# Kernel tuning notes

Measured on AMD Instinct MI355X. Metric: run time of the kernel, lower is better.

The kernel has to match this reference:

```python
import jax, jax.numpy as jnp
import numpy as np

N_NODES = 100000
N_EDGES = 1600000
DIM_IN = 128
DIM_OUT = 128


def setup_inputs() -> dict:
    key = jax.random.key(0)
    k1, k2, k3, k4, k5 = jax.random.split(key, 5)
    x = jax.random.normal(k1, (N_NODES, DIM_IN), dtype=jnp.float32)
    # Dense kernel (glorot-style scale)
    W = jax.random.normal(k2, (DIM_IN, DIM_OUT), dtype=jnp.float32) * (1.0 / np.sqrt(DIM_IN))
    edge_vals = jax.random.uniform(k3, (N_EDGES,), dtype=jnp.float32)
    edge_rows = jax.random.randint(k4, (N_EDGES,), 0, N_NODES, dtype=jnp.int32)
    edge_cols = jax.random.randint(k5, (N_EDGES,), 0, N_NODES, dtype=jnp.int32)
    return {"x": x, "W": W, "edge_vals": edge_vals,
            "edge_rows": edge_rows, "edge_cols": edge_cols}


def reference(x, W, edge_vals, edge_rows, edge_cols):
    # Dense projection (Dense, use_bias=False): [N, dim_in] @ [dim_in, dim_out]
    h = x @ W
    # Sparse adjacency SpMM in COO form:
    # out[r] = sum_{edges e with row r} vals[e] * h[col[e]]
    msgs = edge_vals[:, None] * h[edge_cols]            # [E, dim_out]
    out = jax.ops.segment_sum(msgs, edge_rows, num_segments=N_NODES)
    return out
```

## Files before the change

### kernel.cpp

```cpp
#include <hip/hip_runtime.h>
#include <hip/hip_bf16.h>
#include <hip/hip_fp16.h>


#define DIM 128
#define RB 128
#define NB_MAX 1024
#define CH 4096
#define REG_CAP 2560

typedef short s16x8 __attribute__((ext_vector_type(8)));
typedef float f32x4 __attribute__((ext_vector_type(4)));
typedef unsigned short u16;
typedef unsigned long long u64;
typedef u16 u16x4 __attribute__((ext_vector_type(4)));
typedef u16 u16x8 __attribute__((ext_vector_type(8)));

static __device__ __forceinline__ u16 f2bf(float f) {
  union { float f; unsigned u; } a; a.f = f;
  return (u16)((a.u + 0x7fffu + ((a.u >> 16) & 1u)) >> 16);
}
static __device__ __forceinline__ float bf_lo(unsigned u) {
  union { unsigned u; float f; } a; a.u = u << 16; return a.f;
}
static __device__ __forceinline__ float bf_hi(unsigned u) {
  union { unsigned u; float f; } a; a.u = u & 0xffff0000u; return a.f;
}
static __device__ __forceinline__ u16 f2h(float f) {
  return __half_as_ushort(__float2half(f));
}
static __device__ __forceinline__ float h2f(u16 h) {
  return __half2float(__ushort_as_half(h));
}

__global__ __launch_bounds__(256) void repack_w_kernel(
    const float* __restrict__ W, u16* __restrict__ Wp) {
  int e = blockIdx.x * 256 + threadIdx.x;
  int k = e >> 7, n = e & 127;
  Wp[((k >> 3) * 128 + n) * 8 + (k & 7)] = f2bf(W[e]);
}

__global__ __launch_bounds__(256) void mfma_gemm_kernel(
    const float* __restrict__ x, const u16* __restrict__ Wp,
    u16* __restrict__ hb, int n_nodes) {
  __shared__ u16 xl[128 * 136];
  const int t = threadIdx.x;
  const int m0 = blockIdx.x * 128;

  const float4* x4 = (const float4*)x;
#pragma unroll
  for (int it = 0; it < 16; ++it) {
    int i = it * 256 + t;
    int r = i >> 5, c = i & 31;
    float4 v = make_float4(0.f, 0.f, 0.f, 0.f);
    int node = m0 + r;
    if (node < n_nodes) v = x4[(size_t)node * 32 + c];
    u16x4 pk = {f2bf(v.x), f2bf(v.y), f2bf(v.z), f2bf(v.w)};
    *(u16x4*)&xl[r * 136 + c * 4] = pk;
  }
  __syncthreads();

  const int w = t >> 6, l = t & 63, q = l >> 4, n15 = l & 15;

  f32x4 acc[2][8];
#pragma unroll
  for (int mt = 0; mt < 2; ++mt)
#pragma unroll
    for (int nt = 0; nt < 8; ++nt) acc[mt][nt] = (f32x4){0.f, 0.f, 0.f, 0.f};

#pragma unroll
  for (int ks = 0; ks < 4; ++ks) {
    s16x8 a0 = *(const s16x8*)&xl[(w * 32 + n15) * 136 + ks * 32 + q * 8];
    s16x8 a1 = *(const s16x8*)&xl[(w * 32 + 16 + n15) * 136 + ks * 32 + q * 8];
#pragma unroll
    for (int nt = 0; nt < 8; ++nt) {
      s16x8 b = *(const s16x8*)&Wp[(size_t)(((ks * 4 + q) * 128) + nt * 16 + n15) * 8];
      acc[0][nt] = __builtin_amdgcn_mfma_f32_16x16x32_bf16(a0, b, acc[0][nt], 0, 0, 0);
      acc[1][nt] = __builtin_amdgcn_mfma_f32_16x16x32_bf16(a1, b, acc[1][nt], 0, 0, 0);
    }
  }
  __syncthreads();

#pragma unroll
  for (int mt = 0; mt < 2; ++mt)
#pragma unroll
    for (int nt = 0; nt < 8; ++nt)
#pragma unroll
      for (int r_ = 0; r_ < 4; ++r_)
        xl[(w * 32 + mt * 16 + q * 4 + r_) * 136 + nt * 16 + n15] =
            f2bf(acc[mt][nt][r_]);
  __syncthreads();

#pragma unroll
  for (int it = 0; it < 8; ++it) {
    int chunk = it * 256 + t;
    int r = chunk >> 4, c = chunk & 15;
    int node = m0 + r;
    if (node < n_nodes)
      *(u16x8*)(hb + (size_t)node * 128 + c * 8) = *(const u16x8*)&xl[r * 136 + c * 8];
  }
}

__global__ __launch_bounds__(256) void part_kernel(
    const int* __restrict__ rows, const int* __restrict__ cols,
    const float* __restrict__ vals, int* __restrict__ gcur,
    u64* __restrict__ reg, int n_edges, int nb) {
  __shared__ int hist[NB_MAX];
  __shared__ int ofs[NB_MAX];
  __shared__ int gbase[NB_MAX];
  __shared__ int lcur[NB_MAX];
  __shared__ int tsum[256];
  __shared__ u64 srec[CH];

  const int t = threadIdx.x;
  const int base = blockIdx.x * CH;

  for (int i = t; i < NB_MAX; i += 256) { hist[i] = 0; lcur[i] = 0; }
  __syncthreads();

  int r[16], c[16];
  float v[16];
  bool ok[16];
#pragma unroll
  for (int i = 0; i < 16; ++i) {
    int e = base + i * 256 + t;
    ok[i] = e < n_edges;
    r[i] = ok[i] ? rows[e] : 0;
    c[i] = ok[i] ? cols[e] : 0;
    v[i] = ok[i] ? vals[e] : 0.f;
    if (ok[i]) atomicAdd(&hist[r[i] >> 7], 1);
  }
  __syncthreads();

  const int b0 = t * 4;
  int h0 = hist[b0], h1 = hist[b0 + 1], h2 = hist[b0 + 2], h3 = hist[b0 + 3];
  int run = h0 + h1 + h2 + h3;
  tsum[t] = run;
  for (int b = t; b < nb; b += 256) {
    int hc = hist[b];
    gbase[b] = (hc > 0) ? atomicAdd(&gcur[b], hc) : 0;
  }
  __syncthreads();
  for (int off = 1; off < 256; off <<= 1) {
    int x = (t >= off) ? tsum[t - off] : 0;
    __syncthreads();
    tsum[t] += x;
    __syncthreads();
  }
  int ex = tsum[t] - run;
  ofs[b0] = ex;
  ofs[b0 + 1] = ex + h0;
  ofs[b0 + 2] = ex + h0 + h1;
  ofs[b0 + 3] = ex + h0 + h1 + h2;
  __syncthreads();

#pragma unroll
  for (int i = 0; i < 16; ++i) {
    if (ok[i]) {
      int bkt = r[i] >> 7;
      int pos = ofs[bkt] + atomicAdd(&lcur[bkt], 1);
      srec[pos] = ((u64)(unsigned)r[i] << 33) | ((u64)(unsigned)c[i] << 16) |
                  (u64)f2h(v[i]);
    }
  }
  __syncthreads();

  int nvalid = n_edges - base;
  if (nvalid > CH) nvalid = CH;
  for (int i = t; i < nvalid; i += 256) {
    u64 rec = srec[i];
    int row = (int)(rec >> 33);
    int bkt = row >> 7;
    int dst = gbase[bkt] + (i - ofs[bkt]);
    if (dst < REG_CAP) reg[(size_t)bkt * REG_CAP + dst] = rec;
  }
}

__global__ __launch_bounds__(1024) void bucket_accum_kernel(
    const u16* __restrict__ hb, const u64* __restrict__ reg,
    const int* __restrict__ gcur, float* __restrict__ out, int n_nodes) {
  __shared__ int hist[RB];
  __shared__ int ofs[RB];
  __shared__ int lcur[RB];
  __shared__ u64 srt[REG_CAP];

  const int t = threadIdx.x;
  const int b = blockIdx.x;
  const int row0 = b * RB;

  int n_e = gcur[b];
  if (n_e > REG_CAP) n_e = REG_CAP;

  if (t < RB) { hist[t] = 0; lcur[t] = 0; }
  __syncthreads();

  u64 rr[3];
  int rl[3];
  bool ok[3];
#pragma unroll
  for (int i = 0; i < 3; ++i) {
    int j = i * 1024 + t;
    ok[i] = j < n_e;
    rr[i] = ok[i] ? reg[(size_t)b * REG_CAP + j] : 0;
    rl[i] = (int)(rr[i] >> 33) & (RB - 1);
    if (ok[i]) atomicAdd(&hist[rl[i]], 1);
  }
  __syncthreads();

  if (t < 64) {
    int h0 = hist[2 * t], h1 = hist[2 * t + 1];
    int s = h0 + h1;
    int v = s;
#pragma unroll
    for (int off = 1; off < 64; off <<= 1) {
      int u = __shfl_up(v, off, 64);
      if (t >= off) v += u;
    }
    int ex = v - s;
    ofs[2 * t] = ex;
    ofs[2 * t + 1] = ex + h0;
  }
  __syncthreads();

#pragma unroll
  for (int i = 0; i < 3; ++i) {
    if (ok[i]) {
      int pos = ofs[rl[i]] + atomicAdd(&lcur[rl[i]], 1);
      srt[pos] = rr[i];
    }
  }
  __syncthreads();

  const int lane = t & 63;
  const int w = t >> 6;
  const unsigned* h32 = (const unsigned*)hb;
  float2* out2 = (float2*)out;

  for (int k = 0; k < RB / 16; ++k) {
    int rli = w * (RB / 16) + k;
    int gr = row0 + rli;
    if (gr >= n_nodes) continue;
    int s = ofs[rli];
    int n = hist[rli];
    float2 acc = make_float2(0.f, 0.f);
    int i = 0;
    for (; i + 8 <= n; i += 8) {
      unsigned uu[8];
      float vv[8];
#pragma unroll
      for (int j = 0; j < 8; ++j) {
        u64 rec = srt[s + i + j];
        int col = (int)((rec >> 16) & 0x1FFFF);
        vv[j] = h2f((u16)(rec & 0xFFFF));
        uu[j] = h32[(size_t)col * 64 + lane];
      }
#pragma unroll
      for (int j = 0; j < 8; ++j) {
        acc.x += vv[j] * bf_lo(uu[j]);
        acc.y += vv[j] * bf_hi(uu[j]);
      }
    }
    for (; i < n; ++i) {
      u64 rec = srt[s + i];
      int col = (int)((rec >> 16) & 0x1FFFF);
      float vv = h2f((u16)(rec & 0xFFFF));
      unsigned uu = h32[(size_t)col * 64 + lane];
      acc.x += vv * bf_lo(uu);
      acc.y += vv * bf_hi(uu);
    }
    out2[(size_t)gr * 64 + lane] = acc;
  }
}

__global__ __launch_bounds__(256) void scatter_kernel(
    const u16* __restrict__ hb, const float* __restrict__ vals,
    const int* __restrict__ rows, const int* __restrict__ cols,
    float* __restrict__ out, int n_edges) {
  const int lane = threadIdx.x & 63;
  const int wid = (blockIdx.x * blockDim.x + threadIdx.x) >> 6;
  const int nwaves = (gridDim.x * blockDim.x) >> 6;
  const unsigned* h32 = (const unsigned*)hb;
  for (int e = wid; e < n_edges; e += nwaves) {
    int r = rows[e];
    int c = cols[e];
    float v = vals[e];
    unsigned u = h32[(size_t)c * 64 + lane];
    float* op = out + (size_t)r * DIM + 2 * lane;
    atomicAdd(op, v * bf_lo(u));
    atomicAdd(op + 1, v * bf_hi(u));
  }
}

extern "C" void kernel_launch(void* const* d_in, const int* in_sizes, int n_in,
                              void* d_out, int out_size, void* d_ws, size_t ws_size,
                              hipStream_t stream) {
  const float* x = (const float*)d_in[0];
  const float* W = (const float*)d_in[1];
  const float* edge_vals = (const float*)d_in[2];
  const int* edge_rows = (const int*)d_in[3];
  const int* edge_cols = (const int*)d_in[4];
  float* out = (float*)d_out;

  const int n_nodes = in_sizes[0] / DIM;
  const int n_edges = in_sizes[2];
  const int nb = (n_nodes + RB - 1) / RB;

  char* p = (char*)d_ws;
  u16* hb = (u16*)p;   p += (((size_t)n_nodes * DIM * 2 + 15) / 16) * 16;
  u16* Wp = (u16*)p;   p += (size_t)DIM * DIM * 2;
  int* gcur = (int*)p; p += (((size_t)nb * 4 + 15) / 16) * 16;
  u64* reg = (u64*)p;  p += (size_t)nb * REG_CAP * 8;
  const size_t need = (size_t)(p - (char*)d_ws);

  repack_w_kernel<<<64, 256, 0, stream>>>(W, Wp);
  mfma_gemm_kernel<<<(n_nodes + 127) / 128, 256, 0, stream>>>(x, Wp, hb, n_nodes);

  if (ws_size < need || nb > NB_MAX) {
    hipMemsetAsync(d_out, 0, (size_t)out_size * sizeof(float), stream);
    scatter_kernel<<<2048, 256, 0, stream>>>(hb, edge_vals, edge_rows, edge_cols,
                                             out, n_edges);
    return;
  }

  hipMemsetAsync(gcur, 0, (size_t)nb * sizeof(int), stream);

  int p1_blocks = (n_edges + CH - 1) / CH;
  part_kernel<<<p1_blocks, 256, 0, stream>>>(edge_rows, edge_cols, edge_vals,
                                             gcur, reg, n_edges, nb);

  bucket_accum_kernel<<<nb, 1024, 0, stream>>>(hb, reg, gcur, out, n_nodes);
}
```

Before: 224.5 us.

## Fuse GEMM and edge partition into one launch; pipeline bucket accumulation loads

The dense bf16 GEMM and the edge-bucketing partition now run as one heterogeneous kernel. Blocks are interleaved so GEMM and partition work run on the GPU at the same time, which also removes one launch. The accumulate kernel now treats each wave's eight rows as one contiguous run of edges. It double-buffers the 8-record gather batches so the next batch's loads are in flight while the current one is consumed, and flushes each row's sum when the row index changes. It also adds an occupancy hint to launch bounds and explicitly zeroes rows that have no edges. The risk is extra register pressure from the double buffering, plus branchy flush logic inside the inner loop.

```diff
diff --git a/kernel.cpp b/kernel.cpp
--- a/kernel.cpp
+++ b/kernel.cpp
@@ -40,12 +40,10 @@
   Wp[((k >> 3) * 128 + n) * 8 + (k & 7)] = f2bf(W[e]);
 }
 
-__global__ __launch_bounds__(256) void mfma_gemm_kernel(
+static __device__ __forceinline__ void gemm_body(
     const float* __restrict__ x, const u16* __restrict__ Wp,
-    u16* __restrict__ hb, int n_nodes) {
-  __shared__ u16 xl[128 * 136];
+    u16* __restrict__ hb, int n_nodes, int m0, u16* xl) {
   const int t = threadIdx.x;
-  const int m0 = blockIdx.x * 128;
 
   const float4* x4 = (const float4*)x;
 #pragma unroll
@@ -101,19 +99,12 @@
   }
 }
 
-__global__ __launch_bounds__(256) void part_kernel(
+static __device__ __forceinline__ void part_body(
     const int* __restrict__ rows, const int* __restrict__ cols,
     const float* __restrict__ vals, int* __restrict__ gcur,
-    u64* __restrict__ reg, int n_edges, int nb) {
-  __shared__ int hist[NB_MAX];
-  __shared__ int ofs[NB_MAX];
-  __shared__ int gbase[NB_MAX];
-  __shared__ int lcur[NB_MAX];
-  __shared__ int tsum[256];
-  __shared__ u64 srec[CH];
-
+    u64* __restrict__ reg, int n_edges, int nb, int base,
+    int* hist, int* ofs, int* gbase, int* lcur, int* tsum, u64* srec) {
   const int t = threadIdx.x;
-  const int base = blockIdx.x * CH;
 
   for (int i = t; i < NB_MAX; i += 256) { hist[i] = 0; lcur[i] = 0; }
   __syncthreads();
@@ -142,9 +133,9 @@
   }
   __syncthreads();
   for (int off = 1; off < 256; off <<= 1) {
-    int x = (t >= off) ? tsum[t - off] : 0;
+    int x2 = (t >= off) ? tsum[t - off] : 0;
     __syncthreads();
-    tsum[t] += x;
+    tsum[t] += x2;
     __syncthreads();
   }
   int ex = tsum[t] - run;
@@ -176,7 +167,83 @@
   }
 }
 
-__global__ __launch_bounds__(1024) void bucket_accum_kernel(
+__global__ __launch_bounds__(256) void gemm_part_kernel(
+    const float* __restrict__ x, const u16* __restrict__ Wp, u16* __restrict__ hb,
+    const int* __restrict__ rows, const int* __restrict__ cols,
+    const float* __restrict__ vals, int* __restrict__ gcur, u64* __restrict__ reg,
+    int n_nodes, int n_edges, int nb, int gA, int gP) {
+  __shared__ union {
+    u16 xl[128 * 136];
+    struct {
+      int hist[NB_MAX];
+      int ofs[NB_MAX];
+      int gbase[NB_MAX];
+      int lcur[NB_MAX];
+      int tsum[256];
+      u64 srec[CH];
+    } p;
+  } sh;
+
+  int bid = blockIdx.x;
+  bool isP;
+  int id;
+  if (gA == 2 * gP) {
+    int r = bid % 3, q = bid / 3;
+    isP = (r == 2);
+    id = isP ? q : q * 2 + r;
+  } else {
+    isP = bid < gP;
+    id = isP ? bid : bid - gP;
+  }
+
+  if (!isP) {
+    gemm_body(x, Wp, hb, n_nodes, id * 128, sh.xl);
+  } else {
+    part_body(rows, cols, vals, gcur, reg, n_edges, nb, id * CH,
+              sh.p.hist, sh.p.ofs, sh.p.gbase, sh.p.lcur, sh.p.tsum, sh.p.srec);
+  }
+}
+
+__global__ __launch_bounds__(256) void mfma_gemm_kernel(
+    const float* __restrict__ x, const u16* __restrict__ Wp,
+    u16* __restrict__ hb, int n_nodes) {
+  __shared__ u16 xl[128 * 136];
+  gemm_body(x, Wp, hb, n_nodes, blockIdx.x * 128, xl);
+}
+
+static __device__ __forceinline__ void gload8(
+    const u64* __restrict__ srt, int p, int s1, const unsigned* __restrict__ h32,
+    int lane, unsigned mv[8], unsigned uu[8]) {
+#pragma unroll
+  for (int j = 0; j < 8; ++j) {
+    int idx = p + j;
+    bool vb = idx < s1;
+    idx = vb ? idx : s1 - 1;
+    u64 rec = srt[idx];
+    int col = (int)((rec >> 16) & 0x1FFFF);
+    unsigned val = vb ? (unsigned)(rec & 0xFFFF) : 0u;
+    mv[j] = ((unsigned)((rec >> 33) & (RB - 1)) << 16) | val;
+    uu[j] = h32[((unsigned)col << 6) | lane];
+  }
+}
+static __device__ __forceinline__ void gcons8(
+    const unsigned mv[8], const unsigned uu[8], int& cur, float2& acc,
+    float2* __restrict__ out2, int row0, int lane) {
+#pragma unroll
+  for (int j = 0; j < 8; ++j) {
+    int lr = (int)(mv[j] >> 16);
+    if (lr != cur) {
+      out2[(size_t)(row0 + cur) * 64 + lane] = acc;
+      acc = make_float2(0.f, 0.f);
+      cur = lr;
+    }
+    float vv = h2f((u16)(mv[j] & 0xFFFF));
+    acc.x += vv * bf_lo(uu[j]);
+    acc.y += vv * bf_hi(uu[j]);
+  }
+}
+
+__global__ __launch_bounds__(1024, 8) void bucket_accum_kernel(
     const u16* __restrict__ hb, const u64* __restrict__ reg,
     const int* __restrict__ gcur, float* __restrict__ out, int n_nodes) {
   __shared__ int hist[RB];
@@ -236,39 +303,39 @@
   const unsigned* h32 = (const unsigned*)hb;
   float2* out2 = (float2*)out;
 
-  for (int k = 0; k < RB / 16; ++k) {
-    int rli = w * (RB / 16) + k;
+  const int r0 = w * 8;
+
+#pragma unroll
+  for (int k = 0; k < 8; ++k) {
+    int rli = r0 + k;
     int gr = row0 + rli;
-    if (gr >= n_nodes) continue;
-    int s = ofs[rli];
-    int n = hist[rli];
+    if (gr < n_nodes && hist[rli] == 0)
+      out2[(size_t)gr * 64 + lane] = make_float2(0.f, 0.f);
+  }
+
+  int s0 = ofs[r0];
+  int s1 = ofs[r0 + 7] + hist[r0 + 7];
+  if (s1 > s0) {
     float2 acc = make_float2(0.f, 0.f);
-    int i = 0;
-    for (; i + 8 <= n; i += 8) {
-      unsigned uu[8];
-      float vv[8];
-#pragma unroll
-      for (int j = 0; j < 8; ++j) {
-        u64 rec = srt[s + i + j];
-        int col = (int)((rec >> 16) & 0x1FFFF);
-        vv[j] = h2f((u16)(rec & 0xFFFF));
-        uu[j] = h32[(size_t)col * 64 + lane];
+    int cur = (int)(srt[s0] >> 33) & (RB - 1);
+    unsigned mvA[8], uuA[8], mvB[8], uuB[8];
+    int nbt = (s1 - s0 + 7) >> 3;
+    int p = s0;
+    gload8(srt, p, s1, h32, lane, mvA, uuA);
+    p += 8;
+    for (int bi = 1; bi < nbt; ++bi) {
+      if (bi & 1) {
+        gload8(srt, p, s1, h32, lane, mvB, uuB);
+        gcons8(mvA, uuA, cur, acc, out2, row0, lane);
+      } else {
+        gload8(srt, p, s1, h32, lane, mvA, uuA);
+        gcons8(mvB, uuB, cur, acc, out2, row0, lane);
       }
-#pragma unroll
-      for (int j = 0; j < 8; ++j) {
-        acc.x += vv[j] * bf_lo(uu[j]);
-        acc.y += vv[j] * bf_hi(uu[j]);
-      }
-    }
-    for (; i < n; ++i) {
-      u64 rec = srt[s + i];
-      int col = (int)((rec >> 16) & 0x1FFFF);
-      float vv = h2f((u16)(rec & 0xFFFF));
-      unsigned uu = h32[(size_t)col * 64 + lane];
-      acc.x += vv * bf_lo(uu);
-      acc.y += vv * bf_hi(uu);
-    }
-    out2[(size_t)gr * 64 + lane] = acc;
+      p += 8;
+    }
+    if (nbt & 1) gcons8(mvA, uuA, cur, acc, out2, row0, lane);
+    else gcons8(mvB, uuB, cur, acc, out2, row0, lane);
+    out2[(size_t)(row0 + cur) * 64 + lane] = acc;
   }
 }
 
@@ -313,9 +380,9 @@
   const size_t need = (size_t)(p - (char*)d_ws);
 
   repack_w_kernel<<<64, 256, 0, stream>>>(W, Wp);
-  mfma_gemm_kernel<<<(n_nodes + 127) / 128, 256, 0, stream>>>(x, Wp, hb, n_nodes);
 
   if (ws_size < need || nb > NB_MAX) {
+    mfma_gemm_kernel<<<(n_nodes + 127) / 128, 256, 0, stream>>>(x, Wp, hb, n_nodes);
     hipMemsetAsync(d_out, 0, (size_t)out_size * sizeof(float), stream);
     scatter_kernel<<<2048, 256, 0, stream>>>(hb, edge_vals, edge_rows, edge_cols,
                                              out, n_edges);
@@ -324,9 +391,11 @@
 
   hipMemsetAsync(gcur, 0, (size_t)nb * sizeof(int), stream);
 
-  int p1_blocks = (n_edges + CH - 1) / CH;
-  part_kernel<<<p1_blocks, 256, 0, stream>>>(edge_rows, edge_cols, edge_vals,
-                                             gcur, reg, n_edges, nb);
+  const int gA = (n_nodes + 127) / 128;
+  const int gP = (n_edges + CH - 1) / CH;
+  gemm_part_kernel<<<gA + gP, 256, 0, stream>>>(x, Wp, hb, edge_rows, edge_cols,
+                                                edge_vals, gcur, reg, n_nodes,
+                                                n_edges, nb, gA, gP);
 
   bucket_accum_kernel<<<nb, 1024, 0, stream>>>(hb, reg, gcur, out, n_nodes);
 }
```

Result: slower. 388.2 us (+72.9%).
